# Kernel optimization log

Measured on AMD Instinct MI355X. Metric: run time of the kernel, lower is better.

Reference implementation:

```python
import jax, jax.numpy as jnp
import numpy as np

D = 64      # in_features
U = 1024    # hidden units
B = 4096    # batch

def _build_masks():
    d0 = np.arange(D)
    dh = np.arange(U) % (D - 1)
    m0 = (d0[None, :] <= dh[:, None]).astype(np.float32)          # [U, D]
    m1 = (dh[None, :] <= dh[:, None]).astype(np.float32)          # [U, U]
    m2 = np.tile((dh[None, :] < d0[:, None]).astype(np.float32), (2, 1))  # [2D, U]
    return jnp.asarray(m0), jnp.asarray(m1), jnp.asarray(m2)


def setup_inputs() -> dict:
    key = jax.random.key(0)
    ks = jax.random.split(key, 7)
    scale = 0.02  # small init so exp(sigma) stays finite
    return {
        "u": jax.random.normal(ks[0], (B, D), dtype=jnp.float32),
        "W0": jax.random.normal(ks[1], (U, D), dtype=jnp.float32) * scale,
        "b0": jax.random.normal(ks[2], (U,), dtype=jnp.float32) * scale,
        "W1": jax.random.normal(ks[3], (U, U), dtype=jnp.float32) * scale,
        "b1": jax.random.normal(ks[4], (U,), dtype=jnp.float32) * scale,
        "W2": jax.random.normal(ks[5], (2 * D, U), dtype=jnp.float32) * scale,
        "b2": jax.random.normal(ks[6], (2 * D,), dtype=jnp.float32) * scale,
    }


def reference(u, W0, b0, W1, b1, W2, b2):
    m0, m1, m2 = _build_masks()
    mW0, mW1, mW2 = m0 * W0, m1 * W1, m2 * W2  # masked weights (constant across steps)

    def made(x):  # x: [B, D] -> mu, sigma each [B, D]
        h = jax.nn.relu(x @ mW0.T + b0)
        h = jax.nn.relu(h @ mW1.T + b1)
        z = h @ mW2.T + b2
        return z[:, :D], z[:, D:]

    def step(carry, i):
        x, ldj = carry
        mu, sigma = made(x)
        # ordering = arange(D) (sequential, not reversed) => idx == i
        x = x.at[:, i].set(u[:, i] * jnp.exp(sigma[:, i]) + mu[:, i])
        ldj = ldj.at[:, i].set(sigma[:, i])
        return (x, ldj), None

    x0 = jnp.zeros_like(u)
    ldj0 = jnp.zeros_like(u)
    (x, ldj), _ = jax.lax.scan(step, (x0, ldj0), jnp.arange(D))
    log_det_jacobian = jnp.sum(ldj, axis=1, keepdims=True)  # [B, 1]
    return x, log_det_jacobian
```

## Files before the change

### kernel.cpp

```cpp
#include <hip/hip_runtime.h>
#include <hip/hip_bf16.h>

#define BATCH 4096
#define NTHR 512

typedef __attribute__((ext_vector_type(8))) short bf16x8;
typedef __attribute__((ext_vector_type(4))) float f32x4;
typedef __attribute__((ext_vector_type(4))) short short4v;

#define BAR() asm volatile("s_waitcnt lgkmcnt(0)\n\ts_barrier" ::: "memory")

__host__ __device__ __forceinline__ int off1(int g) { return (g <= 16) ? 17 * g : 16 * g + 16; }
__host__ __device__ __forceinline__ int cntg(int g) { return (g < 16) ? 17 : 16; }
__host__ __device__ __forceinline__ int unitOf(int p) {
    int gp, jp;
    if (p < 272) { gp = p / 17; jp = p - gp * 17; }
    else         { gp = (p >> 4) - 1; jp = p & 15; }
    return gp + 63 * jp;
}
__device__ __forceinline__ short f2bf(float f) {
    __hip_bfloat16 h = __float2bfloat16(f);
    return *reinterpret_cast<short*>(&h);
}

__global__ void prep6(const float* __restrict__ W0, const float* __restrict__ b0,
                      const float* __restrict__ W1, const float* __restrict__ b1,
                      const float* __restrict__ W2,
                      short* __restrict__ W1f, short* __restrict__ W2f,
                      short* __restrict__ W0f, float* __restrict__ b1p) {
    __shared__ short ws[16][1024];
    const int b = blockIdx.x, t = threadIdx.x;
    if (b < 72) {
        const bool isW1 = (b < 64);
        const int n = t >> 5;
        int u;
        if (isW1) u = unitOf(b * 16 + n);
        else { const int c = b - 64; u = (n & 1) ? (64 + c * 8 + (n >> 1)) : (c * 8 + (n >> 1)); }
        const float* src = isW1 ? (W1 + (long)u * 1024) : (W2 + (long)u * 1024);
        const int c0 = (t & 31) * 4;
#pragma unroll
        for (int j = 0; j < 8; ++j) {
            int c = c0 + j * 128;
            float4 v = *(const float4*)&src[c];
            short4v sv;
            sv[0] = f2bf(v.x); sv[1] = f2bf(v.y); sv[2] = f2bf(v.z); sv[3] = f2bf(v.w);
            *(short4v*)&ws[n][c] = sv;
        }
        __syncthreads();
#pragma unroll 1
        for (int it = 0; it < 8; ++it) {
            int v = t + it * 512;
            if (v < 4032) {
                int g = v >> 6, lane2 = v & 63;
                int nn = lane2 & 15, aq2 = lane2 >> 4;
                bf16x8 pk;
#pragma unroll
                for (int e = 0; e < 8; ++e) {
                    int k = aq2 * 8 + e;
                    pk[e] = (k < cntg(g)) ? ws[nn][g + 63 * k] : (short)0;
                }
                if (isW1) *(bf16x8*)&W1f[(((long)g * 64 + b) * 64 + lane2) * 8] = pk;
                else      *(bf16x8*)&W2f[(((long)g * 8 + (b - 64)) * 64 + lane2) * 8] = pk;
            }
        }
    } else if (b < 88) {
        const int bb = b - 72;
#pragma unroll 1
        for (int j = 0; j < 16; ++j) {
            int q = t + j * 512;
            if (q < 8064) {
                int idx = bb * 8064 + q;
                int g = idx >> 11, rem = idx & 2047;
                int n2 = rem >> 10, kt = (rem >> 9) & 1, lane2 = (rem >> 3) & 63, e = rem & 7;
                int sl = n2 * 16 + (lane2 & 15);
                int kp = kt * 32 + ((lane2 >> 4) << 3) + e;
                float val = 0.f;
                if (sl < cntg(g)) {
                    int u = unitOf(off1(g) + sl);
                    if (kp == 0) val = b0[u];
                    else if (kp - 1 <= g) val = W0[u * 64 + kp - 1];
                }
                W0f[idx] = f2bf(val);
            }
        }
    } else {
        for (int p = t; p < 1024; p += 512) b1p[p] = b1[unitOf(p)];
    }
}

__global__ __launch_bounds__(NTHR, 2) void made6(
    const float* __restrict__ uin, const float* __restrict__ b2,
    const short* __restrict__ W1f, const short* __restrict__ W2f,
    const short* __restrict__ W0f, const float* __restrict__ b1p,
    float* __restrict__ out) {

    __shared__ __align__(16) short h1g[16][40];
    __shared__ __align__(16) short h2g[16][40];
    __shared__ __align__(16) short xhist[16][80];
    __shared__ __align__(16) float uT[64][16];
    __shared__ __align__(16) float xLs[16][68];
    __shared__ float ldjpart[8][16];

    const int t = threadIdx.x, lane = t & 63, wv = t >> 6;
    const int n = lane & 15, aq = lane >> 4;
    const int rowbase = blockIdx.x * 16;

    {
        int* z1 = (int*)&h1g[0][0];
        for (int idx = t; idx < 16 * 40 / 2; idx += NTHR) z1[idx] = 0;
        int* z2 = (int*)&h2g[0][0];
        for (int idx = t; idx < 16 * 40 / 2; idx += NTHR) z2[idx] = 0;
        int* z3 = (int*)&xhist[0][0];
        for (int idx = t; idx < 16 * 80 / 2; idx += NTHR) z3[idx] = 0;
    }
    if (t < 256) {
        int r = t >> 4, c0 = (t & 15) * 4;
        float4 v = *(const float4*)&uin[(long)(rowbase + r) * 64 + c0];
        uT[c0 + 0][r] = v.x; uT[c0 + 1][r] = v.y; uT[c0 + 2][r] = v.z; uT[c0 + 3][r] = v.w;
    }

    f32x4 acc2[8];
#pragma unroll
    for (int s = 0; s < 8; ++s) {
        float bb = b1p[(wv + 8 * s) * 16 + n];
        acc2[s] = (f32x4){bb, bb, bb, bb};
    }
    f32x4 zacc;
    {
        int pc = wv * 16 + n;
        float bz = b2[(pc >> 1) + 64 * (pc & 1)];
        zacc = (f32x4){bz, bz, bz, bz};
    }

    bf16x8 w1fE[8], w1fO[8], w2fE, w2fO, w0f0, w0f1, w0f2;
#pragma unroll
    for (int s = 0; s < 8; ++s) {
        const int tile = wv + 8 * s;
        w1fO[s] = *(const bf16x8*)&W1f[(((long)0 * 64 + tile) * 64 + lane) * 8];
        w1fE[s] = *(const bf16x8*)&W1f[(((long)1 * 64 + tile) * 64 + lane) * 8];
    }
    w2fO = *(const bf16x8*)&W2f[(((long)0 * 8 + wv) * 64 + lane) * 8];
    w2fE = *(const bf16x8*)&W2f[(((long)1 * 8 + wv) * 64 + lane) * 8];
    {
        const long gb = 8 * wv;
        w0f0 = *(const bf16x8*)&W0f[((gb * 4 + 0) * 64 + lane) * 8];
        w0f1 = *(const bf16x8*)&W0f[((gb * 4 + 1) * 64 + lane) * 8];
        w0f2 = *(const bf16x8*)&W0f[((gb * 4 + 2) * 64 + lane) * 8];
    }

    f32x4 ldjacc = {0.f, 0.f, 0.f, 0.f};
    BAR();
    if (t < 16) xhist[t][0] = (short)0x3F80;
    float ureg[4];
#pragma unroll
    for (int r = 0; r < 4; ++r) ureg[r] = uT[8 * wv + (n >> 1)][aq * 4 + r];

    auto body = [&](int i, bf16x8* w1fS, bf16x8& w2fS) {
        const int g = i - 1;
        if (g >= 0) {
            const int og = off1(g), cg = cntg(g);
            const int tf0 = og >> 4, tfl = (og + cg - 1) >> 4;
            const int s0 = (tf0 > wv) ? ((tf0 - wv + 7) >> 3) : 0;
            if (s0 < 8) {
                const bf16x8 af = *(const bf16x8*)&h1g[n][aq * 8];
#pragma unroll
                for (int s = 0; s < 8; ++s)
                    if (s >= s0)
                        acc2[s] = __builtin_amdgcn_mfma_f32_16x16x32_bf16(af, w1fS[s], acc2[s], 0, 0, 0);
            }
            {
                const int gp = (i + 1 < 63) ? (i + 1) : 62;
                const int tf0p = off1(gp) >> 4;
                const int s0p = (tf0p > wv) ? ((tf0p - wv + 7) >> 3) : 0;
#pragma unroll
                for (int s = 0; s < 8; ++s)
                    if (s >= s0p)
                        w1fS[s] = *(const bf16x8*)&W1f[(((long)gp * 64 + (wv + 8 * s)) * 64 + lane) * 8];
            }
            if (wv == (tf0 & 7)) {
                const int sT = tf0 >> 3;
                const int j = tf0 * 16 + n - og;
                if (j >= 0 && j < cg) {
#pragma unroll
                    for (int r = 0; r < 4; ++r) {
                        float v = acc2[sT][r];
                        h2g[aq * 4 + r][j] = f2bf(v > 0.f ? v : 0.f);
                    }
                }
            }
            if (tfl != tf0 && wv == (tfl & 7)) {
                const int sT = tfl >> 3;
                const int j = tfl * 16 + n - og;
                if (j < cg) {
#pragma unroll
                    for (int r = 0; r < 4; ++r) {
                        float v = acc2[sT][r];
                        h2g[aq * 4 + r][j] = f2bf(v > 0.f ? v : 0.f);
                    }
                }
            }
            if (g == 16 && wv == 0 && n == 0) {
#pragma unroll
                for (int r = 0; r < 4; ++r) h2g[aq * 4 + r][16] = 0;
            }
        }
        BAR();
        if (g >= 0) {
            const bf16x8 af3 = *(const bf16x8*)&h2g[n][aq * 8];
            zacc = __builtin_amdgcn_mfma_f32_16x16x32_bf16(af3, w2fS, zacc, 0, 0, 0);
            const int gp = (i + 1 < 63) ? (i + 1) : 62;
            w2fS = *(const bf16x8*)&W2f[(((long)gp * 8 + wv) * 64 + lane) * 8];
        }
        if (wv == (i >> 3)) {
            const int n0 = 2 * (i & 7);
            f32x4 sgv;
#pragma unroll
            for (int r = 0; r < 4; ++r) sgv[r] = __shfl_xor(zacc[r], 1);
            if (n == n0) {
#pragma unroll
                for (int r = 0; r < 4; ++r) {
                    const float sg = sgv[r], mu = zacc[r];
                    const float x = ureg[r] * __expf(sg) + mu;
                    ldjacc[r] += sg;
                    const int m = aq * 4 + r;
                    xLs[m][i] = x;
                    if (i < 63) xhist[m][i + 1] = f2bf(x);
                }
            }
            if (i < 63) {
                const bf16x8 ax0 = *(const bf16x8*)&xhist[n][aq * 8];
                f32x4 d0 = {0.f, 0.f, 0.f, 0.f};
                d0 = __builtin_amdgcn_mfma_f32_16x16x32_bf16(ax0, w0f0, d0, 0, 0, 0);
                if (i >= 31) {
                    const bf16x8 ax1 = *(const bf16x8*)&xhist[n][32 + aq * 8];
                    d0 = __builtin_amdgcn_mfma_f32_16x16x32_bf16(ax1, w0f1, d0, 0, 0, 0);
                }
                f32x4 d1 = {0.f, 0.f, 0.f, 0.f};
                if (i < 16)
                    d1 = __builtin_amdgcn_mfma_f32_16x16x32_bf16(ax0, w0f2, d1, 0, 0, 0);
#pragma unroll
                for (int r = 0; r < 4; ++r) {
                    float v = d0[r];
                    h1g[aq * 4 + r][n] = f2bf(v > 0.f ? v : 0.f);
                }
                if (n == 0) {
#pragma unroll
                    for (int r = 0; r < 4; ++r) {
                        float v = (i < 16) ? (d1[r] > 0.f ? d1[r] : 0.f) : 0.f;
                        h1g[aq * 4 + r][16] = f2bf(v);
                    }
                }
                if (i + 1 < 63 && ((i + 1) >> 3) == wv) {
                    const long gb = i + 1;
                    w0f0 = *(const bf16x8*)&W0f[((gb * 4 + 0) * 64 + lane) * 8];
                    w0f1 = *(const bf16x8*)&W0f[((gb * 4 + 1) * 64 + lane) * 8];
                    w0f2 = *(const bf16x8*)&W0f[((gb * 4 + 2) * 64 + lane) * 8];
                }
            }
        }
        BAR();
    };

#pragma unroll 1
    for (int i = 0; i < 64; i += 2) {
        body(i, w1fE, w2fE);
        body(i + 1, w1fO, w2fO);
    }

#pragma unroll
    for (int r = 0; r < 4; ++r) {
        float v = ldjacc[r];
        v += __shfl_xor(v, 2);
        v += __shfl_xor(v, 4);
        v += __shfl_xor(v, 8);
        if (n == 0) ldjpart[wv][aq * 4 + r] = v;
    }
    BAR();

    if (t < 256) {
        int r = t >> 4, c = (t & 15) * 4;
        float4 v;
        v.x = xLs[r][c]; v.y = xLs[r][c + 1]; v.z = xLs[r][c + 2]; v.w = xLs[r][c + 3];
        *(float4*)&out[(long)(rowbase + r) * 64 + c] = v;
    }
    if (t < 16) {
        float s = 0.f;
#pragma unroll
        for (int w = 0; w < 8; ++w) s += ldjpart[w][t];
        out[(long)BATCH * 64 + rowbase + t] = s;
    }
}

extern "C" void kernel_launch(void* const* d_in, const int* in_sizes, int n_in,
                              void* d_out, int out_size, void* d_ws, size_t ws_size,
                              hipStream_t stream) {
    (void)in_sizes; (void)n_in; (void)out_size; (void)ws_size;
    const float* u  = (const float*)d_in[0];
    const float* W0 = (const float*)d_in[1];
    const float* b0 = (const float*)d_in[2];
    const float* W1 = (const float*)d_in[3];
    const float* b1 = (const float*)d_in[4];
    const float* W2 = (const float*)d_in[5];
    const float* b2 = (const float*)d_in[6];
    float* out = (float*)d_out;

    short* W1f = (short*)d_ws;
    short* W2f = (short*)((char*)d_ws + 4128768);
    short* W0f = (short*)((char*)d_ws + 4128768 + 516096);
    float* b1p = (float*)((char*)d_ws + 4128768 + 516096 + 258048);

    prep6<<<dim3(89), dim3(512), 0, stream>>>(W0, b0, W1, b1, W2, W1f, W2f, W0f, b1p);
    made6<<<dim3(BATCH / 16), dim3(NTHR), 0, stream>>>(u, b2, W1f, W2f, W0f, b1p, out);
}
```

Baseline: 176.4 us.

## Remove mid-step barrier via double-buffered hidden tiles and contiguous per-wave tile ownership

Restructures the per-step schedule so each wave owns a contiguous range of W1 output tiles, and the publishing wave both writes h2 and immediately runs the output MFMA and sampling itself. Other waves apply the previous step's h2 contribution one step late. The h1/h2 staging buffers are double-buffered, which removes one of the two block barriers per autoregressive step. It also pads the prep kernel's LDS row to avoid bank conflicts. In exchange the ownership logic gets more complex and the deferred accumulation must stay exactly consistent, and waves 1 and 2 carry an extra accumulator and weight register.

```diff
diff --git a/kernel.cpp b/kernel.cpp
--- a/kernel.cpp
+++ b/kernel.cpp
@@ -23,12 +23,12 @@
     return *reinterpret_cast<short*>(&h);
 }
 
-__global__ void prep6(const float* __restrict__ W0, const float* __restrict__ b0,
+__global__ void prep7(const float* __restrict__ W0, const float* __restrict__ b0,
                       const float* __restrict__ W1, const float* __restrict__ b1,
                       const float* __restrict__ W2,
                       short* __restrict__ W1f, short* __restrict__ W2f,
                       short* __restrict__ W0f, float* __restrict__ b1p) {
-    __shared__ short ws[16][1024];
+    __shared__ short ws[16][1032];
     const int b = blockIdx.x, t = threadIdx.x;
     if (b < 72) {
         const bool isW1 = (b < 64);
@@ -88,14 +88,14 @@
     }
 }
 
-__global__ __launch_bounds__(NTHR, 2) void made6(
+__global__ __launch_bounds__(NTHR, 2) void made7(
     const float* __restrict__ uin, const float* __restrict__ b2,
     const short* __restrict__ W1f, const short* __restrict__ W2f,
     const short* __restrict__ W0f, const float* __restrict__ b1p,
     float* __restrict__ out) {
 
-    __shared__ __align__(16) short h1g[16][40];
-    __shared__ __align__(16) short h2g[16][40];
+    __shared__ __align__(16) short h1b[2][16][40];
+    __shared__ __align__(16) short h2b[2][16][40];
     __shared__ __align__(16) short xhist[16][80];
     __shared__ __align__(16) float uT[64][16];
     __shared__ __align__(16) float xLs[16][68];
@@ -106,10 +106,10 @@
     const int rowbase = blockIdx.x * 16;
 
     {
-        int* z1 = (int*)&h1g[0][0];
-        for (int idx = t; idx < 16 * 40 / 2; idx += NTHR) z1[idx] = 0;
-        int* z2 = (int*)&h2g[0][0];
-        for (int idx = t; idx < 16 * 40 / 2; idx += NTHR) z2[idx] = 0;
+        int* z1 = (int*)&h1b[0][0][0];
+        for (int idx = t; idx < 2 * 16 * 40 / 2; idx += NTHR) z1[idx] = 0;
+        int* z2 = (int*)&h2b[0][0][0];
+        for (int idx = t; idx < 2 * 16 * 40 / 2; idx += NTHR) z2[idx] = 0;
         int* z3 = (int*)&xhist[0][0];
         for (int idx = t; idx < 16 * 80 / 2; idx += NTHR) z3[idx] = 0;
     }
@@ -119,10 +119,13 @@
         uT[c0 + 0][r] = v.x; uT[c0 + 1][r] = v.y; uT[c0 + 2][r] = v.z; uT[c0 + 3][r] = v.w;
     }
 
-    f32x4 acc2[8];
-#pragma unroll
-    for (int s = 0; s < 8; ++s) {
-        float bb = b1p[(wv + 8 * s) * 16 + n];
+    const int B = (wv == 0) ? 0 : (wv == 1) ? 7 : (wv == 2) ? 15 : 8 * wv;
+    const int C = (wv == 1 || wv == 2) ? 9 : 8;
+
+    f32x4 acc2[9];
+#pragma unroll
+    for (int s = 0; s < 9; ++s) {
+        float bb = (s < C) ? b1p[(B + s) * 16 + n] : 0.f;
         acc2[s] = (f32x4){bb, bb, bb, bb};
     }
     f32x4 zacc;
@@ -132,15 +135,13 @@
         zacc = (f32x4){bz, bz, bz, bz};
     }
 
-    bf16x8 w1fE[8], w1fO[8], w2fE, w2fO, w0f0, w0f1, w0f2;
-#pragma unroll
-    for (int s = 0; s < 8; ++s) {
-        const int tile = wv + 8 * s;
-        w1fO[s] = *(const bf16x8*)&W1f[(((long)0 * 64 + tile) * 64 + lane) * 8];
-        w1fE[s] = *(const bf16x8*)&W1f[(((long)1 * 64 + tile) * 64 + lane) * 8];
-    }
-    w2fO = *(const bf16x8*)&W2f[(((long)0 * 8 + wv) * 64 + lane) * 8];
-    w2fE = *(const bf16x8*)&W2f[(((long)1 * 8 + wv) * 64 + lane) * 8];
+    bf16x8 w1f[9], w2g, w2gm1, w0f0, w0f1, w0f2;
+#pragma unroll
+    for (int s = 0; s < 9; ++s)
+        if (s < C)
+            w1f[s] = *(const bf16x8*)&W1f[(((long)0 * 64 + (B + s)) * 64 + lane) * 8];
+    w2g = *(const bf16x8*)&W2f[(((long)0 * 8 + wv) * 64 + lane) * 8];
+    w2gm1 = w2g;
     {
         const long gb = 8 * wv;
         w0f0 = *(const bf16x8*)&W0f[((gb * 4 + 0) * 64 + lane) * 8];
@@ -155,76 +156,87 @@
 #pragma unroll
     for (int r = 0; r < 4; ++r) ureg[r] = uT[8 * wv + (n >> 1)][aq * 4 + r];
 
-    auto body = [&](int i, bf16x8* w1fS, bf16x8& w2fS) {
+#pragma unroll 1
+    for (int i = 0; i < 64; ++i) {
         const int g = i - 1;
+        const bool isPub = (wv == (i >> 3));
+
         if (g >= 0) {
-            const int og = off1(g), cg = cntg(g);
-            const int tf0 = og >> 4, tfl = (og + cg - 1) >> 4;
-            const int s0 = (tf0 > wv) ? ((tf0 - wv + 7) >> 3) : 0;
-            if (s0 < 8) {
-                const bf16x8 af = *(const bf16x8*)&h1g[n][aq * 8];
-#pragma unroll
-                for (int s = 0; s < 8; ++s)
-                    if (s >= s0)
-                        acc2[s] = __builtin_amdgcn_mfma_f32_16x16x32_bf16(af, w1fS[s], acc2[s], 0, 0, 0);
-            }
+            const int og = off1(g);
+            const int tf0 = og >> 4;
+            const bf16x8 af1 = *(const bf16x8*)&h1b[(i + 1) & 1][n][aq * 8];
+            const int s0 = tf0 - B;
+#pragma unroll
+            for (int s = 0; s < 9; ++s)
+                if (s < C && s >= s0)
+                    acc2[s] = __builtin_amdgcn_mfma_f32_16x16x32_bf16(af1, w1f[s], acc2[s], 0, 0, 0);
             {
-                const int gp = (i + 1 < 63) ? (i + 1) : 62;
-                const int tf0p = off1(gp) >> 4;
-                const int s0p = (tf0p > wv) ? ((tf0p - wv + 7) >> 3) : 0;
-#pragma unroll
-                for (int s = 0; s < 8; ++s)
-                    if (s >= s0p)
-                        w1fS[s] = *(const bf16x8*)&W1f[(((long)gp * 64 + (wv + 8 * s)) * 64 + lane) * 8];
-            }
-            if (wv == (tf0 & 7)) {
-                const int sT = tf0 >> 3;
-                const int j = tf0 * 16 + n - og;
-                if (j >= 0 && j < cg) {
+                const int gp = (i < 63) ? i : 62;
+                const int s0p = (off1(gp) >> 4) - B;
+#pragma unroll
+                for (int s = 0; s < 9; ++s)
+                    if (s < C && s >= s0p)
+                        w1f[s] = *(const bf16x8*)&W1f[(((long)gp * 64 + (B + s)) * 64 + lane) * 8];
+            }
+            const bool freshedPrev = (wv == ((i - 1) >> 3));
+            if (!isPub && !freshedPrev && g >= 1) {
+                const bf16x8 af2p = *(const bf16x8*)&h2b[(i - 1) & 1][n][aq * 8];
+                zacc = __builtin_amdgcn_mfma_f32_16x16x32_bf16(af2p, w2gm1, zacc, 0, 0, 0);
+            }
+        }
+
+        if (isPub) {
+            if (g >= 0) {
+                const int og = off1(g), cg = cntg(g);
+                const int tf0 = og >> 4, tfl = (og + cg - 1) >> 4;
+                if ((i & 7) == 0 && g >= 1) {
+                    const bf16x8 af2p = *(const bf16x8*)&h2b[(i - 1) & 1][n][aq * 8];
+                    zacc = __builtin_amdgcn_mfma_f32_16x16x32_bf16(af2p, w2gm1, zacc, 0, 0, 0);
+                }
+                {
+                    const int sT = tf0 - B;
+                    const int j = tf0 * 16 + n - og;
+                    if (j >= 0 && j < cg) {
+#pragma unroll
+                        for (int r = 0; r < 4; ++r) {
+                            float v = acc2[sT][r];
+                            h2b[i & 1][aq * 4 + r][j] = f2bf(v > 0.f ? v : 0.f);
+                        }
+                    }
+                }
+                if (tfl != tf0) {
+                    const int sT = tfl - B;
+                    const int j = tfl * 16 + n - og;
+                    if (j < cg) {
+#pragma unroll
+                        for (int r = 0; r < 4; ++r) {
+                            float v = acc2[sT][r];
+                            h2b[i & 1][aq * 4 + r][j] = f2bf(v > 0.f ? v : 0.f);
+                        }
+                    }
+                }
+                if ((g == 16 || g == 17) && n == 0) {
+#pragma unroll
+                    for (int r = 0; r < 4; ++r) h2b[i & 1][aq * 4 + r][16] = 0;
+                }
+                const bf16x8 af2 = *(const bf16x8*)&h2b[i & 1][n][aq * 8];
+                zacc = __builtin_amdgcn_mfma_f32_16x16x32_bf16(af2, w2g, zacc, 0, 0, 0);
+            }
+            {
+                const int n0 = 2 * (i & 7);
+                f32x4 sgv;
+#pragma unroll
+                for (int r = 0; r < 4; ++r) sgv[r] = __shfl_xor(zacc[r], 1);
+                if (n == n0) {
 #pragma unroll
                     for (int r = 0; r < 4; ++r) {
-                        float v = acc2[sT][r];
-                        h2g[aq * 4 + r][j] = f2bf(v > 0.f ? v : 0.f);
+                        const float sg = sgv[r], mu = zacc[r];
+                        const float x = ureg[r] * __expf(sg) + mu;
+                        ldjacc[r] += sg;
+                        const int m = aq * 4 + r;
+                        xLs[m][i] = x;
+                        if (i < 63) xhist[m][i + 1] = f2bf(x);
                     }
-                }
-            }
-            if (tfl != tf0 && wv == (tfl & 7)) {
-                const int sT = tfl >> 3;
-                const int j = tfl * 16 + n - og;
-                if (j < cg) {
-#pragma unroll
-                    for (int r = 0; r < 4; ++r) {
-                        float v = acc2[sT][r];
-                        h2g[aq * 4 + r][j] = f2bf(v > 0.f ? v : 0.f);
-                    }
-                }
-            }
-            if (g == 16 && wv == 0 && n == 0) {
-#pragma unroll
-                for (int r = 0; r < 4; ++r) h2g[aq * 4 + r][16] = 0;
-            }
-        }
-        BAR();
-        if (g >= 0) {
-            const bf16x8 af3 = *(const bf16x8*)&h2g[n][aq * 8];
-            zacc = __builtin_amdgcn_mfma_f32_16x16x32_bf16(af3, w2fS, zacc, 0, 0, 0);
-            const int gp = (i + 1 < 63) ? (i + 1) : 62;
-            w2fS = *(const bf16x8*)&W2f[(((long)gp * 8 + wv) * 64 + lane) * 8];
-        }
-        if (wv == (i >> 3)) {
-            const int n0 = 2 * (i & 7);
-            f32x4 sgv;
-#pragma unroll
-            for (int r = 0; r < 4; ++r) sgv[r] = __shfl_xor(zacc[r], 1);
-            if (n == n0) {
-#pragma unroll
-                for (int r = 0; r < 4; ++r) {
-                    const float sg = sgv[r], mu = zacc[r];
-                    const float x = ureg[r] * __expf(sg) + mu;
-                    ldjacc[r] += sg;
-                    const int m = aq * 4 + r;
-                    xLs[m][i] = x;
-                    if (i < 63) xhist[m][i + 1] = f2bf(x);
                 }
             }
             if (i < 63) {
@@ -241,13 +253,13 @@
 #pragma unroll
                 for (int r = 0; r < 4; ++r) {
                     float v = d0[r];
-                    h1g[aq * 4 + r][n] = f2bf(v > 0.f ? v : 0.f);
+                    h1b[i & 1][aq * 4 + r][n] = f2bf(v > 0.f ? v : 0.f);
                 }
                 if (n == 0) {
 #pragma unroll
                     for (int r = 0; r < 4; ++r) {
                         float v = (i < 16) ? (d1[r] > 0.f ? d1[r] : 0.f) : 0.f;
-                        h1g[aq * 4 + r][16] = f2bf(v);
+                        h1b[i & 1][aq * 4 + r][16] = f2bf(v);
                     }
                 }
                 if (i + 1 < 63 && ((i + 1) >> 3) == wv) {
@@ -258,13 +270,13 @@
                 }
             }
         }
+
+        w2gm1 = w2g;
+        {
+            const int gz = (i < 63) ? i : 62;
+            w2g = *(const bf16x8*)&W2f[(((long)gz * 8 + wv) * 64 + lane) * 8];
+        }
         BAR();
-    };
-
-#pragma unroll 1
-    for (int i = 0; i < 64; i += 2) {
-        body(i, w1fE, w2fE);
-        body(i + 1, w1fO, w2fO);
     }
 
 #pragma unroll
@@ -309,6 +321,6 @@
     short* W0f = (short*)((char*)d_ws + 4128768 + 516096);
     float* b1p = (float*)((char*)d_ws + 4128768 + 516096 + 258048);
 
-    prep6<<<dim3(89), dim3(512), 0, stream>>>(W0, b0, W1, b1, W2, W1f, W2f, W0f, b1p);
-    made6<<<dim3(BATCH / 16), dim3(NTHR), 0, stream>>>(u, b2, W1f, W2f, W0f, b1p, out);
-}
+    prep7<<<dim3(89), dim3(512), 0, stream>>>(W0, b0, W1, b1, W2, W1f, W2f, W0f, b1p);
+    made7<<<dim3(BATCH / 16), dim3(NTHR), 0, stream>>>(u, b2, W1f, W2f, W0f, b1p, out);
+}
```

After: 212.6 us. 20.5% more time.
